# Kernel optimization log

Measured on AMD Instinct MI355X. Metric: run time of the kernel, lower is better.

Reference implementation:

```python
import jax, jax.numpy as jnp
import numpy as np

B, N, C, H = 4, 1024, 768, 12
D = C // H
SCALE = D ** -0.5


def setup_inputs() -> dict:
    key = jax.random.key(0)
    k1, k2, k3, k4 = jax.random.split(key, 4)
    x1 = jax.random.normal(k1, (B, N, C), dtype=jnp.float32)
    x2 = jax.random.normal(k2, (B, N, C), dtype=jnp.float32)
    # shared (dual-stream) Linear2 weights, torch nn.Linear layout: [out, in]
    W_qkv = jax.random.normal(k3, (3 * C, C), dtype=jnp.float32) * (C ** -0.5)
    b_qkv = jnp.zeros((3 * C,), dtype=jnp.float32)
    W_proj = jax.random.normal(k4, (C, C), dtype=jnp.float32) * (C ** -0.5)
    b_proj = jnp.zeros((C,), dtype=jnp.float32)
    return {"x1": x1, "x2": x2, "W_qkv": W_qkv, "b_qkv": b_qkv,
            "W_proj": W_proj, "b_proj": b_proj}


def _split_qkv(x, W_qkv, b_qkv):
    qkv = (x @ W_qkv.T + b_qkv).reshape(B, N, 3, H, D)
    qkv = jnp.transpose(qkv, (2, 0, 3, 1, 4))  # [3,B,H,N,D]
    return qkv[0], qkv[1], qkv[2]


def reference(x1, x2, W_qkv, b_qkv, W_proj, b_proj):
    q1, k1, v1 = _split_qkv(x1, W_qkv, b_qkv)
    q2, k2, v2 = _split_qkv(x2, W_qkv, b_qkv)
    # two score maps, combined before a single shared softmax
    s1 = jnp.einsum("bhqd,bhkd->bhqk", q1 * SCALE, k1)
    s2 = jnp.einsum("bhqd,bhkd->bhqk", q2 * SCALE, k2)
    attn = jax.nn.softmax(s1 + s2, axis=-1)  # [B,H,N,N]
    # same attention matrix applied to both value streams
    o1 = jnp.einsum("bhqk,bhkd->bhqd", attn, v1)
    o2 = jnpum = jnp.einsum("bhqk,bhkd->bhqd", attn, v2) if False else jnp.einsum("bhqk,bhkd->bhqd", attn, v2)
    o1 = jnp.transpose(o1, (0, 2, 1, 3)).reshape(B, N, C)
    o2 = jnp.transpose(o2, (0, 2, 1, 3)).reshape(B, N, C)
    y1 = o1 @ W_proj.T + b_proj
    y2 = o2 @ W_proj.T + b_proj
    return y1, y2
```

## Files before the change

kernel.cpp:

```cpp
#include <hip/hip_runtime.h>
#include <hip/hip_bf16.h>


typedef __bf16 bf16x8 __attribute__((ext_vector_type(8)));
typedef __bf16 bf16x4 __attribute__((ext_vector_type(4)));
typedef float  f32x4  __attribute__((ext_vector_type(4)));

__device__ __forceinline__ bf16x8 cvt8(const float* p) {
    f32x4 f0 = *(const f32x4*)p;
    f32x4 f1 = *(const f32x4*)(p + 4);
    bf16x8 r;
    r[0] = (__bf16)f0[0]; r[1] = (__bf16)f0[1]; r[2] = (__bf16)f0[2]; r[3] = (__bf16)f0[3];
    r[4] = (__bf16)f1[0]; r[5] = (__bf16)f1[1]; r[6] = (__bf16)f1[2]; r[7] = (__bf16)f1[3];
    return r;
}

__device__ __forceinline__ void async16(const __bf16* g, __bf16* l) {
    __builtin_amdgcn_global_load_lds(
        (const __attribute__((address_space(1))) void*)g,
        (__attribute__((address_space(3))) void*)l, 16, 0, 0);
}

__global__ __launch_bounds__(256)
void cvt3_k(const float* __restrict__ x1, const float* __restrict__ x2,
            const float* __restrict__ wq, __bf16* __restrict__ xc,
            __bf16* __restrict__ wqc)
{
    int bid = blockIdx.x;
    const float* src; __bf16* dst; int i;
    if (bid < 1536)      { src = x1; dst = xc;             i = (bid * 256 + threadIdx.x) * 8; }
    else if (bid < 3072) { src = x2; dst = xc + 3145728;   i = ((bid - 1536) * 256 + threadIdx.x) * 8; }
    else                 { src = wq; dst = wqc;            i = ((bid - 3072) * 256 + threadIdx.x) * 8; }
    *(bf16x8*)(dst + i) = cvt8(src + i);
}

__global__ __launch_bounds__(256)
void cvt_k(const float* __restrict__ src, __bf16* __restrict__ dst, int n) {
    int i = (blockIdx.x * 256 + threadIdx.x) * 8;
    if (i < n) *(bf16x8*)(dst + i) = cvt8(src + i);
}

__global__ __launch_bounds__(256)
void gemm_qkv_s(const __bf16* __restrict__ Xc, const __bf16* __restrict__ Wq,
                const float* __restrict__ bias,
                __bf16* __restrict__ qo, __bf16* __restrict__ ko,
                __bf16* __restrict__ vo)
{
    constexpr int K = 768;
    __shared__ __bf16 As[128 * 32];
    __shared__ __bf16 Bs[128 * 32];

    const int t = threadIdx.x, w = t >> 6, lane = t & 63;
    const int l15 = lane & 15, quad = lane >> 4;
    const int wm = w >> 1, wn = w & 1;

    const int bid  = blockIdx.x;
    const int xcd  = bid & 7;
    const int i6   = bid >> 3;
    const int pair = i6 / 18;
    const int gx   = i6 - pair * 18;
    const int p    = xcd * 8 + pair;
    const int gy   = p & 31;
    const int st   = p >> 5;

    const int lrow = lane >> 2, lcol = (lane & 3) * 8;

    const __bf16* Ab = Xc + (size_t)st * 3145728 + (size_t)(gy * 128) * K;
    const __bf16* Bb = Wq + (size_t)(gx * 128) * K;

    f32x4 acc[4][4];
#pragma unroll
    for (int mi = 0; mi < 4; mi++)
#pragma unroll
        for (int ni = 0; ni < 4; ni++) acc[mi][ni] = f32x4{0.f, 0.f, 0.f, 0.f};

    for (int k0 = 0; k0 < K; k0 += 32) {
#pragma unroll
        for (int i = 0; i < 2; i++) {
            int r = w * 32 + i * 16 + lrow;
            async16(Ab + (size_t)r * K + k0 + lcol, &As[r * 32 + lcol]);
            async16(Bb + (size_t)r * K + k0 + lcol, &Bs[r * 32 + lcol]);
        }
        __syncthreads();
        bf16x8 af[4], bfr[4];
#pragma unroll
        for (int mi = 0; mi < 4; mi++)
            af[mi] = *(const bf16x8*)&As[(wm * 64 + mi * 16 + l15) * 32 + quad * 8];
#pragma unroll
        for (int ni = 0; ni < 4; ni++)
            bfr[ni] = *(const bf16x8*)&Bs[(wn * 64 + ni * 16 + l15) * 32 + quad * 8];
#pragma unroll
        for (int mi = 0; mi < 4; mi++)
#pragma unroll
            for (int ni = 0; ni < 4; ni++)
                acc[mi][ni] = __builtin_amdgcn_mfma_f32_16x16x32_bf16(af[mi], bfr[ni], acc[mi][ni], 0, 0, 0);
        __syncthreads();
    }

    const int which = (gx * 128) / 768;

    if (which == 2) {
#pragma unroll
        for (int ni = 0; ni < 4; ni++) {
            int j = gx * 128 + wn * 64 + ni * 16 + l15;
            int c = j - 1536;
            int h = c >> 6, d = c & 63;
            float bj = bias[j];
#pragma unroll
            for (int mi = 0; mi < 4; mi++) {
                int row0 = gy * 128 + wm * 64 + mi * 16 + quad * 4;
                int b = row0 >> 10, tok0 = row0 & 1023;
                bf16x4 pv;
#pragma unroll
                for (int r = 0; r < 4; r++) pv[r] = (__bf16)(acc[mi][ni][r] + bj);
                *(bf16x4*)&vo[((size_t)((st * 4 + b) * 12 + h) * 64 + d) * 1024 + tok0] = pv;
            }
        }
    } else {
#pragma unroll
        for (int ni = 0; ni < 4; ni++) {
            int j     = gx * 128 + wn * 64 + ni * 16 + l15;
            int c     = j - which * 768;
            int h = c >> 6, d = c & 63;
            float bj  = bias[j];
#pragma unroll
            for (int mi = 0; mi < 4; mi++) {
#pragma unroll
                for (int r = 0; r < 4; r++) {
                    int row = gy * 128 + wm * 64 + mi * 16 + quad * 4 + r;
                    int b = row >> 10, tok = row & 1023;
                    float val = acc[mi][ni][r] + bj;
                    if (which == 0)
                        qo[((size_t)((st * 4 + b) * 12 + h) * 1024 + tok) * 64 + d] = (__bf16)(val * 0.125f);
                    else
                        ko[((size_t)((st * 4 + b) * 12 + h) * 1024 + tok) * 64 + d] = (__bf16)val;
                }
            }
        }
    }
}

__global__ __launch_bounds__(256)
void gemm_proj(const __bf16* __restrict__ A, const __bf16* __restrict__ Wp,
               const float* __restrict__ bias, float* __restrict__ out)
{
    constexpr int K = 768;
    __shared__ __bf16 As[128 * 32];
    __shared__ __bf16 Bs[128 * 32];

    const int t = threadIdx.x, w = t >> 6, lane = t & 63;
    const int l15 = lane & 15, quad = lane >> 4;
    const int wm = w >> 1, wn = w & 1;
    const int gx = blockIdx.x, gy = blockIdx.y;
    const int lrow = lane >> 2, lcol = (lane & 3) * 8;

    const __bf16* Ab = A  + (size_t)(gy * 128) * K;
    const __bf16* Bb = Wp + (size_t)(gx * 128) * K;

    f32x4 acc[4][4];
#pragma unroll
    for (int mi = 0; mi < 4; mi++)
#pragma unroll
        for (int ni = 0; ni < 4; ni++) acc[mi][ni] = f32x4{0.f, 0.f, 0.f, 0.f};

    for (int k0 = 0; k0 < K; k0 += 32) {
#pragma unroll
        for (int i = 0; i < 2; i++) {
            int r = w * 32 + i * 16 + lrow;
            async16(Ab + (size_t)r * K + k0 + lcol, &As[r * 32 + lcol]);
            async16(Bb + (size_t)r * K + k0 + lcol, &Bs[r * 32 + lcol]);
        }
        __syncthreads();
        bf16x8 af[4], bfr[4];
#pragma unroll
        for (int mi = 0; mi < 4; mi++)
            af[mi] = *(const bf16x8*)&As[(wm * 64 + mi * 16 + l15) * 32 + quad * 8];
#pragma unroll
        for (int ni = 0; ni < 4; ni++)
            bfr[ni] = *(const bf16x8*)&Bs[(wn * 64 + ni * 16 + l15) * 32 + quad * 8];
#pragma unroll
        for (int mi = 0; mi < 4; mi++)
#pragma unroll
            for (int ni = 0; ni < 4; ni++)
                acc[mi][ni] = __builtin_amdgcn_mfma_f32_16x16x32_bf16(af[mi], bfr[ni], acc[mi][ni], 0, 0, 0);
        __syncthreads();
    }

#pragma unroll
    for (int ni = 0; ni < 4; ni++) {
        int col  = gx * 128 + wn * 64 + ni * 16 + l15;
        float bj = bias[col];
#pragma unroll
        for (int mi = 0; mi < 4; mi++)
#pragma unroll
            for (int r = 0; r < 4; r++) {
                int row = gy * 128 + wm * 64 + mi * 16 + quad * 4 + r;
                out[(size_t)row * 768 + col] = acc[mi][ni][r] + bj;
            }
    }
}

__global__ __launch_bounds__(256)
void attn_k(const __bf16* __restrict__ qws, const __bf16* __restrict__ kws,
            const __bf16* __restrict__ vws, __bf16* __restrict__ ows)
{
    __shared__ __bf16 KVf[2][2][2][2][4][512];
    __shared__ __bf16 Ps[4][16 * 72];

    const int g  = blockIdx.x;
    const int qt = g / 48;
    const int bh = g % 48;
    const int b = bh / 12, h = bh % 12;
    const int t = threadIdx.x, w = t >> 6, lane = t & 63;
    const int l15 = lane & 15, quad = lane >> 4;

    const size_t head_off = (size_t)bh * 65536;
    const size_t ss       = (size_t)48 * 65536;

    bf16x8 qf[2][2];
#pragma unroll
    for (int s = 0; s < 2; s++)
#pragma unroll
        for (int kk = 0; kk < 2; kk++)
            qf[s][kk] = *(const bf16x8*)(qws + s * ss + head_off
                          + (size_t)(qt * 64 + w * 16 + l15) * 64 + kk * 32 + quad * 8);

    float lsum = 0.f;
    f32x4 accO[2][4];
#pragma unroll
    for (int s = 0; s < 2; s++)
#pragma unroll
        for (int mi = 0; mi < 4; mi++) accO[s][mi] = f32x4{0.f, 0.f, 0.f, 0.f};

    const __bf16* kbase = kws + head_off;
    const __bf16* vbase = vws + head_off;

    for (int kt2 = 0; kt2 < 8; kt2++) {
        __syncthreads();
#pragma unroll
        for (int i = 0; i < 16; i++) {
            int f    = w * 16 + i;
            int tile = f >> 5, rem = f & 31;
            int kv = rem >> 4, s = (rem >> 3) & 1, kk = (rem >> 2) & 1, mi = rem & 3;
            int keyb = kt2 * 128 + tile * 64;
            const __bf16* gp;
            if (kv == 0)
                gp = kbase + s * ss + (size_t)(keyb + mi * 16 + l15) * 64
                     + kk * 32 + quad * 8;
            else
                gp = vbase + s * ss + (size_t)(mi * 16 + l15) * 1024
                     + keyb + kk * 32 + quad * 8;
            async16(gp, &KVf[tile][kv][s][kk][mi][lane * 8]);
        }
        __syncthreads();

#pragma unroll
        for (int tile = 0; tile < 2; tile++) {
            f32x4 accS[4];
#pragma unroll
            for (int i = 0; i < 4; i++) accS[i] = f32x4{0.f, 0.f, 0.f, 0.f};
#pragma unroll
            for (int s = 0; s < 2; s++)
#pragma unroll
                for (int kk = 0; kk < 2; kk++) {
                    bf16x8 kf[4];
#pragma unroll
                    for (int mi = 0; mi < 4; mi++)
                        kf[mi] = *(const bf16x8*)&KVf[tile][0][s][kk][mi][lane * 8];
#pragma unroll
                    for (int mi = 0; mi < 4; mi++)
                        accS[mi] = __builtin_amdgcn_mfma_f32_16x16x32_bf16(kf[mi], qf[s][kk], accS[mi], 0, 0, 0);
                }

            float rs = 0.f;
            bf16x4 pk[4];
#pragma unroll
            for (int mi = 0; mi < 4; mi++)
#pragma unroll
                for (int r = 0; r < 4; r++) {
                    float pv = __expf(accS[mi][r]);
                    pk[mi][r] = (__bf16)pv;
                    rs += pv;
                }
            lsum += rs;

#pragma unroll
            for (int mi = 0; mi < 4; mi++)
                *(bf16x4*)&Ps[w][l15 * 72 + mi * 16 + quad * 4] = pk[mi];

#pragma unroll
            for (int kk = 0; kk < 2; kk++) {
                bf16x8 pa = *(const bf16x8*)&Ps[w][l15 * 72 + kk * 32 + quad * 8];
#pragma unroll
                for (int s = 0; s < 2; s++)
#pragma unroll
                    for (int mi = 0; mi < 4; mi++) {
                        bf16x8 vf = *(const bf16x8*)&KVf[tile][1][s][kk][mi][lane * 8];
                        accO[s][mi] = __builtin_amdgcn_mfma_f32_16x16x32_bf16(vf, pa, accO[s][mi], 0, 0, 0);
                    }
            }
        }
    }

    lsum += __shfl_xor(lsum, 16);
    lsum += __shfl_xor(lsum, 32);
    float il = 1.f / lsum;

    const int tok = qt * 64 + w * 16 + l15;
#pragma unroll
    for (int s = 0; s < 2; s++)
#pragma unroll
        for (int mi = 0; mi < 4; mi++) {
            bf16x4 ov;
#pragma unroll
            for (int r = 0; r < 4; r++) ov[r] = (__bf16)(accO[s][mi][r] * il);
            *(bf16x4*)&ows[((size_t)((s * 4 + b) * 1024 + tok)) * 768
                           + h * 64 + mi * 16 + quad * 4] = ov;
        }
}

extern "C" void kernel_launch(void* const* d_in, const int* in_sizes, int n_in,
                              void* d_out, int out_size, void* d_ws, size_t ws_size,
                              hipStream_t stream)
{
    const float* x1    = (const float*)d_in[0];
    const float* x2    = (const float*)d_in[1];
    const float* Wqkv  = (const float*)d_in[2];
    const float* bqkv  = (const float*)d_in[3];
    const float* Wproj = (const float*)d_in[4];
    const float* bproj = (const float*)d_in[5];
    float* out = (float*)d_out;

    const size_t qkv_elems = (size_t)2 * 4 * 12 * 1024 * 64;
    __bf16* q_ws = (__bf16*)d_ws;
    __bf16* k_ws = q_ws + qkv_elems;
    __bf16* v_ws = k_ws + qkv_elems;
    __bf16* pool = v_ws + qkv_elems;
    __bf16* Wqc  = pool + 3145728;
    __bf16* o_ws = pool;
    __bf16* Wpc  = q_ws;
    __bf16* Xc   = (__bf16*)d_out;

    cvt3_k<<<3936, 256, 0, stream>>>(x1, x2, Wqkv, Xc, Wqc);
    gemm_qkv_s<<<1152, 256, 0, stream>>>(Xc, Wqc, bqkv, q_ws, k_ws, v_ws);
    attn_k<<<768, 256, 0, stream>>>(q_ws, k_ws, v_ws, o_ws);
    cvt_k<<<288, 256, 0, stream>>>(Wproj, Wpc, 589824);
    gemm_proj<<<dim3(6, 64), 256, 0, stream>>>(o_ws, Wpc, bproj, out);
}
```

Measured before the change: 228.9 us.

## Double-buffer K/V tiles in attention with async prefetch of next tile

Replaces the load-then-compute loop over 128-key chunks with a 64-key double-buffered pipeline. While the current tile is consumed, each wave issues async global-to-LDS loads for the next tile, then syncs once per iteration. MFMA sections are wrapped in s_setprio to favour matrix issue. This hides global load latency behind compute at the cost of more iterations and a barrier per 64 keys.

```diff
diff --git a/kernel.cpp b/kernel.cpp
--- a/kernel.cpp
+++ b/kernel.cpp
@@ -204,7 +204,7 @@
 void attn_k(const __bf16* __restrict__ qws, const __bf16* __restrict__ kws,
             const __bf16* __restrict__ vws, __bf16* __restrict__ ows)
 {
-    __shared__ __bf16 KVf[2][2][2][2][4][512];
+    __shared__ __bf16 KV[2][2][2][2][4][512];
     __shared__ __bf16 Ps[4][16 * 72];
 
     const int g  = blockIdx.x;
@@ -232,74 +232,84 @@
 #pragma unroll
         for (int mi = 0; mi < 4; mi++) accO[s][mi] = f32x4{0.f, 0.f, 0.f, 0.f};
 
-    const __bf16* kbase = kws + head_off;
-    const __bf16* vbase = vws + head_off;
-
-    for (int kt2 = 0; kt2 < 8; kt2++) {
-        __syncthreads();
-#pragma unroll
-        for (int i = 0; i < 16; i++) {
-            int f    = w * 16 + i;
-            int tile = f >> 5, rem = f & 31;
-            int kv = rem >> 4, s = (rem >> 3) & 1, kk = (rem >> 2) & 1, mi = rem & 3;
-            int keyb = kt2 * 128 + tile * 64;
-            const __bf16* gp;
-            if (kv == 0)
-                gp = kbase + s * ss + (size_t)(keyb + mi * 16 + l15) * 64
-                     + kk * 32 + quad * 8;
-            else
-                gp = vbase + s * ss + (size_t)(mi * 16 + l15) * 1024
-                     + keyb + kk * 32 + quad * 8;
-            async16(gp, &KVf[tile][kv][s][kk][mi][lane * 8]);
-        }
-        __syncthreads();
-
-#pragma unroll
-        for (int tile = 0; tile < 2; tile++) {
-            f32x4 accS[4];
-#pragma unroll
-            for (int i = 0; i < 4; i++) accS[i] = f32x4{0.f, 0.f, 0.f, 0.f};
+    const int skv = w >> 1, sst = w & 1;
+    const __bf16* sbase = (skv ? vws : kws) + head_off + (size_t)sst * ss;
+
+#pragma unroll
+    for (int i = 0; i < 8; i++) {
+        const int kk = i >> 2, mi = i & 3;
+        const __bf16* gp = skv
+            ? sbase + (size_t)(mi * 16 + l15) * 1024 + kk * 32 + quad * 8
+            : sbase + (size_t)(mi * 16 + l15) * 64 + kk * 32 + quad * 8;
+        async16(gp, &KV[0][skv][sst][kk][mi][lane * 8]);
+    }
+    __syncthreads();
+
+#pragma unroll 2
+    for (int kt = 0; kt < 16; kt++) {
+        const int cb = kt & 1, nb = cb ^ 1;
+
+        if (kt < 15) {
+            const int keyb = (kt + 1) * 64;
+#pragma unroll
+            for (int i = 0; i < 8; i++) {
+                const int kk = i >> 2, mi = i & 3;
+                const __bf16* gp = skv
+                    ? sbase + (size_t)(mi * 16 + l15) * 1024 + keyb + kk * 32 + quad * 8
+                    : sbase + (size_t)(keyb + mi * 16 + l15) * 64 + kk * 32 + quad * 8;
+                async16(gp, &KV[nb][skv][sst][kk][mi][lane * 8]);
+            }
+        }
+
+        f32x4 accS[4];
+#pragma unroll
+        for (int i = 0; i < 4; i++) accS[i] = f32x4{0.f, 0.f, 0.f, 0.f};
+        __builtin_amdgcn_s_setprio(1);
+#pragma unroll
+        for (int s = 0; s < 2; s++)
+#pragma unroll
+            for (int kk = 0; kk < 2; kk++) {
+                bf16x8 kf[4];
+#pragma unroll
+                for (int mi = 0; mi < 4; mi++)
+                    kf[mi] = *(const bf16x8*)&KV[cb][0][s][kk][mi][lane * 8];
+#pragma unroll
+                for (int mi = 0; mi < 4; mi++)
+                    accS[mi] = __builtin_amdgcn_mfma_f32_16x16x32_bf16(kf[mi], qf[s][kk], accS[mi], 0, 0, 0);
+            }
+        __builtin_amdgcn_s_setprio(0);
+
+        float rs = 0.f;
+        bf16x4 pk[4];
+#pragma unroll
+        for (int mi = 0; mi < 4; mi++)
+#pragma unroll
+            for (int r = 0; r < 4; r++) {
+                float pv = __expf(accS[mi][r]);
+                pk[mi][r] = (__bf16)pv;
+                rs += pv;
+            }
+        lsum += rs;
+
+#pragma unroll
+        for (int mi = 0; mi < 4; mi++)
+            *(bf16x4*)&Ps[w][l15 * 72 + mi * 16 + quad * 4] = pk[mi];
+
+        __builtin_amdgcn_s_setprio(1);
+#pragma unroll
+        for (int kk = 0; kk < 2; kk++) {
+            bf16x8 pa = *(const bf16x8*)&Ps[w][l15 * 72 + kk * 32 + quad * 8];
 #pragma unroll
             for (int s = 0; s < 2; s++)
 #pragma unroll
-                for (int kk = 0; kk < 2; kk++) {
-                    bf16x8 kf[4];
-#pragma unroll
-                    for (int mi = 0; mi < 4; mi++)
-                        kf[mi] = *(const bf16x8*)&KVf[tile][0][s][kk][mi][lane * 8];
-#pragma unroll
-                    for (int mi = 0; mi < 4; mi++)
-                        accS[mi] = __builtin_amdgcn_mfma_f32_16x16x32_bf16(kf[mi], qf[s][kk], accS[mi], 0, 0, 0);
+                for (int mi = 0; mi < 4; mi++) {
+                    bf16x8 vf = *(const bf16x8*)&KV[cb][1][s][kk][mi][lane * 8];
+                    accO[s][mi] = __builtin_amdgcn_mfma_f32_16x16x32_bf16(vf, pa, accO[s][mi], 0, 0, 0);
                 }
-
-            float rs = 0.f;
-            bf16x4 pk[4];
-#pragma unroll
-            for (int mi = 0; mi < 4; mi++)
-#pragma unroll
-                for (int r = 0; r < 4; r++) {
-                    float pv = __expf(accS[mi][r]);
-                    pk[mi][r] = (__bf16)pv;
-                    rs += pv;
-                }
-            lsum += rs;
-
-#pragma unroll
-            for (int mi = 0; mi < 4; mi++)
-                *(bf16x4*)&Ps[w][l15 * 72 + mi * 16 + quad * 4] = pk[mi];
-
-#pragma unroll
-            for (int kk = 0; kk < 2; kk++) {
-                bf16x8 pa = *(const bf16x8*)&Ps[w][l15 * 72 + kk * 32 + quad * 8];
-#pragma unroll
-                for (int s = 0; s < 2; s++)
-#pragma unroll
-                    for (int mi = 0; mi < 4; mi++) {
-                        bf16x8 vf = *(const bf16x8*)&KVf[tile][1][s][kk][mi][lane * 8];
-                        accO[s][mi] = __builtin_amdgcn_mfma_f32_16x16x32_bf16(vf, pa, accO[s][mi], 0, 0, 0);
-                    }
-            }
-        }
+        }
+        __builtin_amdgcn_s_setprio(0);
+
+        __syncthreads();
     }
 
     lsum += __shfl_xor(lsum, 16);
```

Result: no change. 228.3 us (-0.3%).
